# Performance work log

Hardware: AMD Instinct MI355X
Metric: run time of the kernel (lower is better)

## Reference

```python
import jax, jax.numpy as jnp
import numpy as np

N = 50000      # nodes
K = 32         # fixed neighbor count per node
D_IN, D_HID, D_OUT = 512, 128, 64


def setup_inputs() -> dict:
    key = jax.random.key(0)
    k1, k2, k3, k4 = jax.random.split(key, 4)
    feat = jax.random.normal(k1, (N, D_IN), dtype=jnp.float32)
    W1 = jax.random.normal(k2, (D_IN, D_HID), dtype=jnp.float32) * (1.0 / np.sqrt(D_IN))
    b1 = jnp.zeros((D_HID,), dtype=jnp.float32)
    W2 = jax.random.normal(k3, (D_HID, D_OUT), dtype=jnp.float32) * (1.0 / np.sqrt(D_HID))
    b2 = jnp.zeros((D_OUT,), dtype=jnp.float32)
    neighbors = jax.random.randint(k4, (N, K), 0, N, dtype=jnp.int64)
    return {"feat": feat, "W1": W1, "b1": b1, "W2": W2, "b2": b2,
            "neighbors": neighbors}


def _median_conv(x, W, b, neighbors):
    # linear transform, then per-node median over neighbor messages
    h = x @ W + b                      # [N, D]
    nb = h[neighbors]                  # [N, K, D]  gather (irregular access)
    # torch.median returns the lower middle element for even K
    med = jnp.sort(nb, axis=1)[:, (K - 1) // 2]   # [N, D]
    return med


def reference(feat, W1, b1, W2, b2, neighbors):
    # MedianGCN forward (eval mode: dropout is identity), norm='none'
    h = jax.nn.relu(_median_conv(feat, W1, b1, neighbors))
    out = _median_conv(h, W2, b2, neighbors)
    return out
```

## Files before the change

### kernel.cpp

```cpp
#include <hip/hip_runtime.h>
#include <cstddef>

#define NN   50000
#define KNB  32

typedef _Float16 h2    __attribute__((ext_vector_type(2)));
typedef _Float16 h4    __attribute__((ext_vector_type(4)));
typedef _Float16 half8 __attribute__((ext_vector_type(8)));
typedef float    f4    __attribute__((ext_vector_type(4)));

__global__ __launch_bounds__(256) void prep(const float* __restrict__ W1,
                                            const float* __restrict__ W2,
                                            _Float16* __restrict__ w1t,
                                            _Float16* __restrict__ w2t) {
  const int id = blockIdx.x * 256 + threadIdx.x;
  if (id < 128 * 512) {
    const int n = id >> 9, k = id & 511;
    w1t[id] = (_Float16)W1[k * 128 + n];
  } else {
    const int id2 = id - 128 * 512;
    if (id2 < 64 * 128) {
      const int n = id2 >> 7, k = id2 & 127;
      w2t[id2] = (_Float16)W2[k * 64 + n];
    }
  }
}

__global__ __launch_bounds__(256) void gemm1_mfma(
    const float* __restrict__ A, const _Float16* __restrict__ Bt,
    const float* __restrict__ bias, _Float16* __restrict__ C, int M) {
  constexpr int K = 512, BM = 64, BK = 64;
  __shared__ _Float16 Ah[BM][72];
  __shared__ _Float16 Bh[128][72];
  const int tid  = threadIdx.x;
  const int wave = tid >> 6;
  const int lane = tid & 63;
  const int mr   = lane & 15;
  const int kg   = lane >> 4;
  const int m0   = blockIdx.x * BM;

  const int ar = tid >> 4;
  const int ac = (tid & 15) * 4;
  const int br = tid >> 3;
  const int bc = (tid & 7) * 8;

  f4 acc[8] = {};

  for (int k0 = 0; k0 < K; k0 += BK) {
    #pragma unroll
    for (int c = 0; c < 4; ++c) {
      const int arow = c * 16 + ar;
      int aRow = m0 + arow;
      if (aRow >= M) aRow = M - 1;
      const f4 t = *(const f4*)(A + (size_t)aRow * K + k0 + ac);
      h4 hv = {(_Float16)t[0], (_Float16)t[1], (_Float16)t[2], (_Float16)t[3]};
      *(h4*)&Ah[arow][ac] = hv;
      const int brow = c * 32 + br;
      *(half8*)&Bh[brow][bc] =
          *(const half8*)(Bt + (size_t)brow * K + k0 + bc);
    }
    __syncthreads();

    #pragma unroll
    for (int kk = 0; kk < 2; ++kk) {
      const half8 af = *(const half8*)&Ah[wave * 16 + mr][kk * 32 + kg * 8];
      #pragma unroll
      for (int nt = 0; nt < 8; ++nt) {
        const half8 bf = *(const half8*)&Bh[nt * 16 + mr][kk * 32 + kg * 8];
        acc[nt] = __builtin_amdgcn_mfma_f32_16x16x32_f16(af, bf, acc[nt], 0, 0, 0);
      }
    }
    __syncthreads();
  }

  #pragma unroll
  for (int nt = 0; nt < 8; ++nt) {
    const int col = nt * 16 + mr;
    const float bv = bias[col];
    #pragma unroll
    for (int r = 0; r < 4; ++r) {
      const int row = m0 + wave * 16 + kg * 4 + r;
      if (row < M)
        C[(size_t)row * 128 + col] = (_Float16)(acc[nt][r] + bv);
    }
  }
}

__global__ __launch_bounds__(256) void gemm2_mfma(
    const _Float16* __restrict__ A, const _Float16* __restrict__ Bt,
    const float* __restrict__ bias, _Float16* __restrict__ C, int M) {
  constexpr int K = 128, BM = 64, BK = 64;
  __shared__ _Float16 Ah[BM][72];
  __shared__ _Float16 Bh[64][72];
  const int tid  = threadIdx.x;
  const int wave = tid >> 6;
  const int lane = tid & 63;
  const int mr   = lane & 15;
  const int kg   = lane >> 4;
  const int m0   = blockIdx.x * BM;

  const int sr = tid >> 3;
  const int sc = (tid & 7) * 8;

  f4 acc[4] = {};

  #pragma unroll
  for (int k0 = 0; k0 < K; k0 += BK) {
    #pragma unroll
    for (int c = 0; c < 2; ++c) {
      const int srow = c * 32 + sr;
      int aRow = m0 + srow;
      if (aRow >= M) aRow = M - 1;
      *(half8*)&Ah[srow][sc] = *(const half8*)(A + (size_t)aRow * K + k0 + sc);
      *(half8*)&Bh[srow][sc] = *(const half8*)(Bt + (size_t)srow * K + k0 + sc);
    }
    __syncthreads();

    #pragma unroll
    for (int kk = 0; kk < 2; ++kk) {
      const half8 af = *(const half8*)&Ah[wave * 16 + mr][kk * 32 + kg * 8];
      #pragma unroll
      for (int nt = 0; nt < 4; ++nt) {
        const half8 bf = *(const half8*)&Bh[nt * 16 + mr][kk * 32 + kg * 8];
        acc[nt] = __builtin_amdgcn_mfma_f32_16x16x32_f16(af, bf, acc[nt], 0, 0, 0);
      }
    }
    __syncthreads();
  }

  #pragma unroll
  for (int nt = 0; nt < 4; ++nt) {
    const int col = nt * 16 + mr;
    const float bv = bias[col];
    #pragma unroll
    for (int r = 0; r < 4; ++r) {
      const int row = m0 + wave * 16 + kg * 4 + r;
      if (row < M)
        C[(size_t)row * 64 + col] = (_Float16)(acc[nt][r] + bv);
    }
  }
}

__device__ __forceinline__ void ceh(h2& a, h2& b) {
  h2 lo = __builtin_elementwise_min(a, b);
  h2 hi = __builtin_elementwise_max(a, b);
  a = lo;
  b = hi;
}

__device__ __forceinline__ void sort16h(h2 (&v)[16]) {
  #pragma unroll
  for (int p = 1; p < 16; p <<= 1) {
    #pragma unroll
    for (int k = p; k >= 1; k >>= 1) {
      #pragma unroll
      for (int j = k & (p - 1); j + k < 16; j += 2 * k) {
        #pragma unroll
        for (int i = 0; i < k; ++i) {
          if (i + j + k < 16) {
            if ((i + j) / (2 * p) == (i + j + k) / (2 * p)) {
              ceh(v[i + j], v[i + j + k]);
            }
          }
        }
      }
    }
  }
}

__device__ __forceinline__ h2 median32h(h2 (&a)[16], h2 (&b)[16]) {
  sort16h(a);
  sort16h(b);
  h2 m = __builtin_elementwise_min(a[15], b[15]);
  #pragma unroll
  for (int i = 0; i < 15; ++i) {
    m = __builtin_elementwise_min(
        m, __builtin_elementwise_max(a[i], b[14 - i]));
  }
  return m;
}

__global__ __launch_bounds__(256, 4) void median_relu1(
    const _Float16* __restrict__ H, const int* __restrict__ nb,
    _Float16* __restrict__ O) {
  const int lane = threadIdx.x & 63;
  const int node = blockIdx.x * 8 + ((threadIdx.x >> 6) << 1) + (lane >> 5);
  const int col2 = blockIdx.y * 32 + (lane & 31);
  const unsigned coff = (unsigned)col2 * 4u;
  const int4* nrow = (const int4*)(nb + (size_t)node * KNB);
  const char* Hb = (const char*)H;
  h2 a[16], b[16];
  #pragma unroll
  for (int q = 0; q < 4; ++q) {
    const int4 ii = nrow[q];
    a[q * 4 + 0] = *(const h2*)(Hb + (((unsigned)ii.x << 8) + coff));
    a[q * 4 + 1] = *(const h2*)(Hb + (((unsigned)ii.y << 8) + coff));
    a[q * 4 + 2] = *(const h2*)(Hb + (((unsigned)ii.z << 8) + coff));
    a[q * 4 + 3] = *(const h2*)(Hb + (((unsigned)ii.w << 8) + coff));
  }
  #pragma unroll
  for (int q = 0; q < 4; ++q) {
    const int4 ii = nrow[4 + q];
    b[q * 4 + 0] = *(const h2*)(Hb + (((unsigned)ii.x << 8) + coff));
    b[q * 4 + 1] = *(const h2*)(Hb + (((unsigned)ii.y << 8) + coff));
    b[q * 4 + 2] = *(const h2*)(Hb + (((unsigned)ii.z << 8) + coff));
    b[q * 4 + 3] = *(const h2*)(Hb + (((unsigned)ii.w << 8) + coff));
  }
  const h2 med = median32h(a, b);
  const h2 z = (h2)((_Float16)0);
  *(h2*)((char*)O + ((size_t)node * 256 + coff)) =
      __builtin_elementwise_max(med, z);
}

__global__ __launch_bounds__(256, 4) void median2(
    const _Float16* __restrict__ H, const int* __restrict__ nb,
    float2* __restrict__ O) {
  const int node = blockIdx.x * 8 + (threadIdx.x >> 5);
  const int lane = threadIdx.x & 31;
  const unsigned coff = (unsigned)lane * 4u;
  const int4* nrow = (const int4*)(nb + (size_t)node * KNB);
  const char* Hb = (const char*)H;
  h2 a[16], b[16];
  #pragma unroll
  for (int q = 0; q < 4; ++q) {
    const int4 ii = nrow[q];
    a[q * 4 + 0] = *(const h2*)(Hb + (((unsigned)ii.x << 7) + coff));
    a[q * 4 + 1] = *(const h2*)(Hb + (((unsigned)ii.y << 7) + coff));
    a[q * 4 + 2] = *(const h2*)(Hb + (((unsigned)ii.z << 7) + coff));
    a[q * 4 + 3] = *(const h2*)(Hb + (((unsigned)ii.w << 7) + coff));
  }
  #pragma unroll
  for (int q = 0; q < 4; ++q) {
    const int4 ii = nrow[4 + q];
    b[q * 4 + 0] = *(const h2*)(Hb + (((unsigned)ii.x << 7) + coff));
    b[q * 4 + 1] = *(const h2*)(Hb + (((unsigned)ii.y << 7) + coff));
    b[q * 4 + 2] = *(const h2*)(Hb + (((unsigned)ii.z << 7) + coff));
    b[q * 4 + 3] = *(const h2*)(Hb + (((unsigned)ii.w << 7) + coff));
  }
  const h2 med = median32h(a, b);
  float2 o;
  o.x = (float)med[0];
  o.y = (float)med[1];
  O[(size_t)node * 32 + lane] = o;
}

extern "C" void kernel_launch(void* const* d_in, const int* in_sizes, int n_in,
                              void* d_out, int out_size, void* d_ws, size_t ws_size,
                              hipStream_t stream) {
  const float* feat = (const float*)d_in[0];
  const float* W1   = (const float*)d_in[1];
  const float* b1   = (const float*)d_in[2];
  const float* W2   = (const float*)d_in[3];
  const float* b2   = (const float*)d_in[4];
  const int*   nb   = (const int*)d_in[5];
  float* out = (float*)d_out;

  _Float16* h1   = (_Float16*)d_ws;
  _Float16* med1 = h1 + (size_t)NN * 128;
  _Float16* w1t  = med1 + (size_t)NN * 128;
  _Float16* w2t  = w1t + 128 * 512;
  _Float16* h2b  = h1;

  prep<<<dim3(288), dim3(256), 0, stream>>>(W1, W2, w1t, w2t);
  gemm1_mfma<<<dim3((NN + 63) / 64), dim3(256), 0, stream>>>(feat, w1t, b1, h1, NN);
  median_relu1<<<dim3(NN / 8, 2), dim3(256), 0, stream>>>(h1, nb, med1);
  gemm2_mfma<<<dim3((NN + 63) / 64), dim3(256), 0, stream>>>(med1, w2t, b2, h2b, NN);
  median2<<<dim3(NN / 8), dim3(256), 0, stream>>>(h2b, nb, (float2*)out);
}
```

Before: 242.3 us.

## Split each node's 32-neighbor median across two half-waves with shuffle merge

Each node's 32 neighbors are now split between two 32-lane halves of a wavefront. Each half sorts 16 values, and the bitonic-style final merge exchanges elements through cross-half shuffles (xor 32). This halves the per-thread register footprint and sorting work, and doubles the number of threads and blocks, to gain occupancy and latency hiding. In exchange it adds shuffle traffic, leaves half the lanes idle on the store, and drops the occupancy hint in launch_bounds.

After: 636.8 us. +162.8%, slower.

```diff
diff --git a/kernel.cpp b/kernel.cpp
--- a/kernel.cpp
+++ b/kernel.cpp
@@ -168,80 +168,83 @@
   }
 }
 
-__device__ __forceinline__ h2 median32h(h2 (&a)[16], h2 (&b)[16]) {
-  sort16h(a);
-  sort16h(b);
-  h2 m = __builtin_elementwise_min(a[15], b[15]);
+__device__ __forceinline__ h2 shx32(h2 x) {
+  int xi = __builtin_bit_cast(int, x);
+  int r = __shfl_xor(xi, 32, 64);
+  return __builtin_bit_cast(h2, r);
+}
+
+__device__ __forceinline__ h2 median32_pair(h2 (&v)[16], int h) {
+  sort16h(v);
+  h2 m;
   #pragma unroll
   for (int i = 0; i < 15; ++i) {
-    m = __builtin_elementwise_min(
-        m, __builtin_elementwise_max(a[i], b[14 - i]));
-  }
-  return m;
-}
-
-__global__ __launch_bounds__(256, 4) void median_relu1(
+    const h2 own = h ? v[14 - i] : v[i];
+    const h2 rec = shx32(own);
+    const h2 mx = __builtin_elementwise_max(own, rec);
+    m = (i == 0) ? mx : __builtin_elementwise_min(m, mx);
+    if (i == 4 || i == 9)
+      __builtin_amdgcn_sched_barrier(0);
+  }
+  const h2 own15 = v[15];
+  const h2 rec15 = shx32(own15);
+  return __builtin_elementwise_min(
+      m, __builtin_elementwise_min(own15, rec15));
+}
+
+__global__ __launch_bounds__(256) void median_relu1(
     const _Float16* __restrict__ H, const int* __restrict__ nb,
     _Float16* __restrict__ O) {
   const int lane = threadIdx.x & 63;
-  const int node = blockIdx.x * 8 + ((threadIdx.x >> 6) << 1) + (lane >> 5);
+  const int h    = lane >> 5;
+  const int node = blockIdx.x * 4 + (threadIdx.x >> 6);
   const int col2 = blockIdx.y * 32 + (lane & 31);
   const unsigned coff = (unsigned)col2 * 4u;
-  const int4* nrow = (const int4*)(nb + (size_t)node * KNB);
+  const int4* nrow = (const int4*)(nb + (size_t)node * KNB + h * 16);
   const char* Hb = (const char*)H;
-  h2 a[16], b[16];
+  h2 v[16];
   #pragma unroll
   for (int q = 0; q < 4; ++q) {
     const int4 ii = nrow[q];
-    a[q * 4 + 0] = *(const h2*)(Hb + (((unsigned)ii.x << 8) + coff));
-    a[q * 4 + 1] = *(const h2*)(Hb + (((unsigned)ii.y << 8) + coff));
-    a[q * 4 + 2] = *(const h2*)(Hb + (((unsigned)ii.z << 8) + coff));
-    a[q * 4 + 3] = *(const h2*)(Hb + (((unsigned)ii.w << 8) + coff));
-  }
-  #pragma unroll
-  for (int q = 0; q < 4; ++q) {
-    const int4 ii = nrow[4 + q];
-    b[q * 4 + 0] = *(const h2*)(Hb + (((unsigned)ii.x << 8) + coff));
-    b[q * 4 + 1] = *(const h2*)(Hb + (((unsigned)ii.y << 8) + coff));
-    b[q * 4 + 2] = *(const h2*)(Hb + (((unsigned)ii.z << 8) + coff));
-    b[q * 4 + 3] = *(const h2*)(Hb + (((unsigned)ii.w << 8) + coff));
-  }
-  const h2 med = median32h(a, b);
-  const h2 z = (h2)((_Float16)0);
-  *(h2*)((char*)O + ((size_t)node * 256 + coff)) =
-      __builtin_elementwise_max(med, z);
-}
-
-__global__ __launch_bounds__(256, 4) void median2(
+    v[q * 4 + 0] = *(const h2*)(Hb + (((unsigned)ii.x << 8) + coff));
+    v[q * 4 + 1] = *(const h2*)(Hb + (((unsigned)ii.y << 8) + coff));
+    v[q * 4 + 2] = *(const h2*)(Hb + (((unsigned)ii.z << 8) + coff));
+    v[q * 4 + 3] = *(const h2*)(Hb + (((unsigned)ii.w << 8) + coff));
+  }
+  const h2 med = median32_pair(v, h);
+  if (h == 0) {
+    const h2 z = (h2)((_Float16)0);
+    *(h2*)((char*)O + ((size_t)node * 256 + coff)) =
+        __builtin_elementwise_max(med, z);
+  }
+}
+
+__global__ __launch_bounds__(256) void median2(
     const _Float16* __restrict__ H, const int* __restrict__ nb,
     float2* __restrict__ O) {
-  const int node = blockIdx.x * 8 + (threadIdx.x >> 5);
-  const int lane = threadIdx.x & 31;
-  const unsigned coff = (unsigned)lane * 4u;
-  const int4* nrow = (const int4*)(nb + (size_t)node * KNB);
+  const int lane = threadIdx.x & 63;
+  const int h    = lane >> 5;
+  const int node = blockIdx.x * 4 + (threadIdx.x >> 6);
+  const int col2 = lane & 31;
+  const unsigned coff = (unsigned)col2 * 4u;
+  const int4* nrow = (const int4*)(nb + (size_t)node * KNB + h * 16);
   const char* Hb = (const char*)H;
-  h2 a[16], b[16];
+  h2 v[16];
   #pragma unroll
   for (int q = 0; q < 4; ++q) {
     const int4 ii = nrow[q];
-    a[q * 4 + 0] = *(const h2*)(Hb + (((unsigned)ii.x << 7) + coff));
-    a[q * 4 + 1] = *(const h2*)(Hb + (((unsigned)ii.y << 7) + coff));
-    a[q * 4 + 2] = *(const h2*)(Hb + (((unsigned)ii.z << 7) + coff));
-    a[q * 4 + 3] = *(const h2*)(Hb + (((unsigned)ii.w << 7) + coff));
-  }
-  #pragma unroll
-  for (int q = 0; q < 4; ++q) {
-    const int4 ii = nrow[4 + q];
-    b[q * 4 + 0] = *(const h2*)(Hb + (((unsigned)ii.x << 7) + coff));
-    b[q * 4 + 1] = *(const h2*)(Hb + (((unsigned)ii.y << 7) + coff));
-    b[q * 4 + 2] = *(const h2*)(Hb + (((unsigned)ii.z << 7) + coff));
-    b[q * 4 + 3] = *(const h2*)(Hb + (((unsigned)ii.w << 7) + coff));
-  }
-  const h2 med = median32h(a, b);
-  float2 o;
-  o.x = (float)med[0];
-  o.y = (float)med[1];
-  O[(size_t)node * 32 + lane] = o;
+    v[q * 4 + 0] = *(const h2*)(Hb + (((unsigned)ii.x << 7) + coff));
+    v[q * 4 + 1] = *(const h2*)(Hb + (((unsigned)ii.y << 7) + coff));
+    v[q * 4 + 2] = *(const h2*)(Hb + (((unsigned)ii.z << 7) + coff));
+    v[q * 4 + 3] = *(const h2*)(Hb + (((unsigned)ii.w << 7) + coff));
+  }
+  const h2 med = median32_pair(v, h);
+  if (h == 0) {
+    float2 o;
+    o.x = (float)med[0];
+    o.y = (float)med[1];
+    O[(size_t)node * 32 + col2] = o;
+  }
 }
 
 extern "C" void kernel_launch(void* const* d_in, const int* in_sizes, int n_in,
@@ -263,7 +266,7 @@
 
   prep<<<dim3(288), dim3(256), 0, stream>>>(W1, W2, w1t, w2t);
   gemm1_mfma<<<dim3((NN + 63) / 64), dim3(256), 0, stream>>>(feat, w1t, b1, h1, NN);
-  median_relu1<<<dim3(NN / 8, 2), dim3(256), 0, stream>>>(h1, nb, med1);
+  median_relu1<<<dim3(NN / 4, 2), dim3(256), 0, stream>>>(h1, nb, med1);
   gemm2_mfma<<<dim3((NN + 63) / 64), dim3(256), 0, stream>>>(med1, w2t, b2, h2b, NN);
-  median2<<<dim3(NN / 8), dim3(256), 0, stream>>>(h2b, nb, (float2*)out);
-}
+  median2<<<dim3(NN / 4), dim3(256), 0, stream>>>(h2b, nb, (float2*)out);
+}
```
